# Optimization experiments

Measured on AMD Instinct MI355X. Metric: run time of the kernel, lower is better.

## Reference

```python
import jax, jax.numpy as jnp
import numpy as np

BN_EPS = 1e-5

def setup_inputs() -> dict:
    key = jax.random.key(0)
    k1, k2, k3 = jax.random.split(key, 3)
    N, F, H, E = 50000, 256, 256, 1600000
    x = jax.random.normal(k1, (N, F), dtype=jnp.float32)
    edge_index = jax.random.randint(k2, (2, E), 0, N, dtype=jnp.int64)
    # Linear(F, H) params, PyTorch default init scale
    lim = 1.0 / np.sqrt(F)
    W = jax.random.uniform(k3, (H, F), dtype=jnp.float32, minval=-lim, maxval=lim)
    b = jnp.zeros((H,), dtype=jnp.float32)
    bn_w = jnp.ones((H,), dtype=jnp.float32)
    bn_b = jnp.zeros((H,), dtype=jnp.float32)
    return {"x": x, "edge_index": edge_index, "W": W, "b": b, "bn_w": bn_w, "bn_b": bn_b}

def reference(x, edge_index, W, b, bn_w, bn_b):
    N = x.shape[0]
    src, dst = edge_index[0], edge_index[1]
    # GIN aggregation: sum of neighbor features (messages flow src -> dst)
    agg = jax.ops.segment_sum(x[src], dst, num_segments=N)
    h = x + agg  # (1 + eps) * x + agg, eps = 0
    # MLP: Linear then BatchNorm1d (training mode: batch stats, biased var)
    h = jnp.einsum('nf,hf->nh', h, W) + b
    mean = jnp.mean(h, axis=0)
    var = jnp.mean(jnp.square(h - mean), axis=0)
    out = (h - mean) * jax.lax.rsqrt(var + BN_EPS) * bn_w + bn_b
    return out
```

## Files before the change

kernel.cpp:

```cpp
#include <hip/hip_runtime.h>

#define NN 50000
#define FDIM 256
#define HDIM 256
#define BN_EPS 1e-5f
#define RB 32
#define KC 16
#define NP 264
#define SCAN_CHUNK 1024
#define NBLK_SCAN ((NN + SCAN_CHUNK - 1) / SCAN_CHUNK)

#define BKT 32
#define NBKT 1563
#define ECAP 1280
#define PFB2 1024
#define PSC_NPT 7
#define PAIR_SRC(p) (((p) >> 5) & 0xFFFFu)
#define PAIR_LDST(p) ((p) & 31u)

typedef __attribute__((ext_vector_type(8))) short short8v;
typedef __attribute__((ext_vector_type(8))) unsigned short ushort8v;
typedef __attribute__((ext_vector_type(4))) float f32x4;

__device__ __forceinline__ float b2f(unsigned short u) {
    return __uint_as_float(((unsigned)u) << 16);
}
__device__ __forceinline__ unsigned short f2b(float f) {
    unsigned u = __float_as_uint(f);
    return (unsigned short)((u + 0x7FFFu + ((u >> 16) & 1u)) >> 16);
}

__launch_bounds__(256)
__global__ void k_cvthist(const float4* __restrict__ x, const float4* __restrict__ W,
                          ushort4* __restrict__ xb, ushort4* __restrict__ Wb,
                          int nx4, int nw4,
                          const int* __restrict__ dst, int* __restrict__ bcnt, int E) {
    const int bid = blockIdx.x;
    const int t = threadIdx.x;
    if (bid < 256) {
        __shared__ int lhist[NBKT];
        int chunk = (E + 255) / 256;
        int c0 = bid * chunk;
        int c1 = min(E, c0 + chunk);
        for (int i = t; i < NBKT; i += 256) lhist[i] = 0;
        __syncthreads();
        for (int e = c0 + t; e < c1; e += 256) atomicAdd(&lhist[dst[e] >> 5], 1);
        __syncthreads();
        for (int i = t; i < NBKT; i += 256) {
            int h = lhist[i];
            if (h) atomicAdd(&bcnt[i], h);
        }
    } else {
        int i = (bid - 256) * 256 + t;
        if (i < nx4) {
            float4 v = x[i];
            xb[i] = make_ushort4(f2b(v.x), f2b(v.y), f2b(v.z), f2b(v.w));
        } else {
            int j = i - nx4;
            if (j < nw4) {
                float4 v = W[j];
                Wb[j] = make_ushort4(f2b(v.x), f2b(v.y), f2b(v.z), f2b(v.w));
            }
        }
    }
}

__global__ void k_pscan(const int* __restrict__ bcnt, int* __restrict__ bbase,
                        int* __restrict__ bcursor) {
    __shared__ int ts[256];
    int t = threadIdx.x;
    int i0 = t * PSC_NPT;
    int s = 0;
    for (int i = 0; i < PSC_NPT; i++) {
        int idx = i0 + i;
        if (idx < NBKT) s += bcnt[idx];
    }
    ts[t] = s;
    __syncthreads();
    for (int off = 1; off < 256; off <<= 1) {
        int val = (t >= off) ? ts[t - off] : 0;
        __syncthreads();
        ts[t] += val;
        __syncthreads();
    }
    int run = ts[t] - s;
    for (int i = 0; i < PSC_NPT; i++) {
        int idx = i0 + i;
        if (idx < NBKT) {
            bbase[idx] = run;
            bcursor[idx] = run;
            run += bcnt[idx];
        }
    }
}

__launch_bounds__(256)
__global__ void k_pfill(const int* __restrict__ src, const int* __restrict__ dst,
                        int* __restrict__ bcursor, unsigned int* __restrict__ pairs, int E) {
    __shared__ int lhist[NBKT];
    __shared__ int lbase[NBKT];
    int t = threadIdx.x;
    int chunk = (E + PFB2 - 1) / PFB2;
    int c0 = blockIdx.x * chunk;
    int c1 = min(E, c0 + chunk);
    for (int i = t; i < NBKT; i += 256) lhist[i] = 0;
    __syncthreads();
    for (int e = c0 + t; e < c1; e += 256) atomicAdd(&lhist[dst[e] >> 5], 1);
    __syncthreads();
    for (int i = t; i < NBKT; i += 256) {
        int h = lhist[i];
        lbase[i] = h ? atomicAdd(&bcursor[i], h) : 0;
        lhist[i] = 0;
    }
    __syncthreads();
    for (int e = c0 + t; e < c1; e += 256) {
        int d = dst[e];
        unsigned bkt = (unsigned)d >> 5;
        int rank = atomicAdd(&lhist[bkt], 1);
        pairs[lbase[bkt] + rank] = (bkt << 21) | ((unsigned)src[e] << 5) | ((unsigned)d & 31u);
    }
}

__launch_bounds__(256, 6)
__global__ void k_agg_gemm(const ushort4* __restrict__ xb4, const unsigned int* __restrict__ pairs,
                           const int* __restrict__ bbase, const int* __restrict__ bcnt,
                           const unsigned short* __restrict__ Wb, const float* __restrict__ bias,
                           unsigned short* __restrict__ hb, float* __restrict__ stat) {
    __shared__ unsigned int lp[ECAP];
    __shared__ int lhist[BKT];
    __shared__ int lofs[BKT + 1];
    __shared__ unsigned short As[BKT * NP];
    __shared__ float ssum[HDIM];
    __shared__ float ssq[HDIM];
    const int t = threadIdx.x;
    const int lane = t & 63;
    const int wid = t >> 6;
    const int q = lane >> 4;
    const int l16 = lane & 15;
    const int v0 = blockIdx.x * BKT;
    const int ebeg = bbase[blockIdx.x];
    const int ecnt = bcnt[blockIdx.x];
    const int vrows = min(BKT, NN - v0);

    ssum[t] = 0.f;
    ssq[t] = 0.f;

    if (ecnt <= ECAP) {
        if (t < BKT) lhist[t] = 0;
        __syncthreads();
        for (int e = t; e < ecnt; e += 256)
            atomicAdd(&lhist[PAIR_LDST(pairs[ebeg + e])], 1);
        __syncthreads();
        if (t == 0) {
            int run = 0;
            for (int r = 0; r < BKT; r++) { lofs[r] = run; run += lhist[r]; }
            lofs[BKT] = run;
        }
        __syncthreads();
        if (t < BKT) lhist[t] = lofs[t];
        __syncthreads();
        for (int e = t; e < ecnt; e += 256) {
            unsigned int p = pairs[ebeg + e];
            int pos = atomicAdd(&lhist[PAIR_LDST(p)], 1);
            lp[pos] = p;
        }
        __syncthreads();
#pragma unroll
        for (int i = 0; i < 8; i++) {
            int r = wid * 8 + i;
            int v = v0 + r;
            if (v < NN) {
                ushort4 u0 = xb4[(size_t)v * 64 + lane];
                float a0 = b2f(u0.x), a1 = b2f(u0.y), a2 = b2f(u0.z), a3 = b2f(u0.w);
                int e0 = __builtin_amdgcn_readfirstlane(lofs[r]);
                int e1 = __builtin_amdgcn_readfirstlane(lofs[r + 1]);
                int e = e0;
                for (; e + 16 <= e1; e += 16) {
                    ushort4 u[16];
#pragma unroll
                    for (int j = 0; j < 16; j++)
                        u[j] = xb4[(size_t)PAIR_SRC(lp[e + j]) * 64 + lane];
#pragma unroll
                    for (int j = 0; j < 16; j++) {
                        a0 += b2f(u[j].x); a1 += b2f(u[j].y);
                        a2 += b2f(u[j].z); a3 += b2f(u[j].w);
                    }
                }
                for (; e + 4 <= e1; e += 4) {
                    ushort4 ua = xb4[(size_t)PAIR_SRC(lp[e]) * 64 + lane];
                    ushort4 ub = xb4[(size_t)PAIR_SRC(lp[e + 1]) * 64 + lane];
                    ushort4 uc = xb4[(size_t)PAIR_SRC(lp[e + 2]) * 64 + lane];
                    ushort4 ud = xb4[(size_t)PAIR_SRC(lp[e + 3]) * 64 + lane];
                    a0 += (b2f(ua.x) + b2f(ub.x)) + (b2f(uc.x) + b2f(ud.x));
                    a1 += (b2f(ua.y) + b2f(ub.y)) + (b2f(uc.y) + b2f(ud.y));
                    a2 += (b2f(ua.z) + b2f(ub.z)) + (b2f(uc.z) + b2f(ud.z));
                    a3 += (b2f(ua.w) + b2f(ub.w)) + (b2f(uc.w) + b2f(ud.w));
                }
                for (; e < e1; e++) {
                    ushort4 ua = xb4[(size_t)PAIR_SRC(lp[e]) * 64 + lane];
                    a0 += b2f(ua.x); a1 += b2f(ua.y); a2 += b2f(ua.z); a3 += b2f(ua.w);
                }
                *(ushort4*)(As + r * NP + lane * 4) =
                    make_ushort4(f2b(a0), f2b(a1), f2b(a2), f2b(a3));
            } else {
                *(ushort4*)(As + r * NP + lane * 4) = make_ushort4(0, 0, 0, 0);
            }
        }
    } else {
#pragma unroll
        for (int i = 0; i < 8; i++) {
            int r = wid * 8 + i;
            int v = v0 + r;
            float a0 = 0.f, a1 = 0.f, a2 = 0.f, a3 = 0.f;
            if (v < NN) {
                ushort4 u0 = xb4[(size_t)v * 64 + lane];
                a0 = b2f(u0.x); a1 = b2f(u0.y); a2 = b2f(u0.z); a3 = b2f(u0.w);
                for (int e = 0; e < ecnt; e++) {
                    unsigned int p = pairs[ebeg + e];
                    if ((int)PAIR_LDST(p) == r) {
                        ushort4 cu = xb4[(size_t)PAIR_SRC(p) * 64 + lane];
                        a0 += b2f(cu.x); a1 += b2f(cu.y); a2 += b2f(cu.z); a3 += b2f(cu.w);
                    }
                }
            }
            *(ushort4*)(As + r * NP + lane * 4) =
                make_ushort4(f2b(a0), f2b(a1), f2b(a2), f2b(a3));
        }
    }
    __syncthreads();

    f32x4 acc[2][4];
#pragma unroll
    for (int mt = 0; mt < 2; mt++)
#pragma unroll
        for (int nt = 0; nt < 4; nt++) acc[mt][nt] = (f32x4)0.f;

    const int w = wid;
#pragma unroll
    for (int ks = 0; ks < 8; ks++) {
        const int kk = ks * 32;
        short8v af[2], bf_[4];
#pragma unroll
        for (int mt = 0; mt < 2; mt++)
            af[mt] = *(const short8v*)(As + (mt * 16 + l16) * NP + kk + q * 8);
#pragma unroll
        for (int nt = 0; nt < 4; nt++)
            bf_[nt] = *(const short8v*)(Wb + (size_t)(w * 64 + nt * 16 + l16) * FDIM + kk + q * 8);
#pragma unroll
        for (int mt = 0; mt < 2; mt++)
#pragma unroll
            for (int nt = 0; nt < 4; nt++)
                acc[mt][nt] = __builtin_amdgcn_mfma_f32_16x16x32_bf16(af[mt], bf_[nt], acc[mt][nt], 0, 0, 0);
    }

#pragma unroll
    for (int nt = 0; nt < 4; nt++) {
        const int col = w * 64 + nt * 16 + l16;
        const float bcol = bias[col];
        float s = 0.f, qq = 0.f;
#pragma unroll
        for (int mt = 0; mt < 2; mt++) {
            const int rbase = mt * 16 + q * 4;
#pragma unroll
            for (int r = 0; r < 4; r++) {
                int row = rbase + r;
                if (row < vrows) {
                    float v = acc[mt][nt][r] + bcol;
                    hb[(size_t)(v0 + row) * FDIM + col] = f2b(v);
                    s += v;
                    qq += v * v;
                }
            }
        }
        atomicAdd(&ssum[col], s);
        atomicAdd(&ssq[col], qq);
    }
    __syncthreads();
    atomicAdd(&stat[t], ssum[t]);
    atomicAdd(&stat[256 + t], ssq[t]);
}

__global__ void k_final(const float* __restrict__ stat, const float* __restrict__ bn_w,
                        const float* __restrict__ bn_b, float* __restrict__ ss) {
    int j = threadIdx.x;
    const float inv_n = 1.0f / (float)NN;
    float mean = stat[j] * inv_n;
    float var = stat[256 + j] * inv_n - mean * mean;
    float sc = bn_w[j] * rsqrtf(var + BN_EPS);
    ss[j] = sc;
    ss[256 + j] = bn_b[j] - mean * sc;
}

__global__ void k_norm8(const ushort8v* __restrict__ hb8, const float* __restrict__ ss,
                        float4* __restrict__ out, int n8) {
    int i = blockIdx.x * blockDim.x + threadIdx.x;
    if (i >= n8) return;
    ushort8v u = hb8[i];
    int c8 = (i & 31) << 3;
    float4 sc0 = *(const float4*)(ss + c8);
    float4 sc1 = *(const float4*)(ss + c8 + 4);
    float4 sh0 = *(const float4*)(ss + 256 + c8);
    float4 sh1 = *(const float4*)(ss + 256 + c8 + 4);
    float4 v0, v1;
    v0.x = fmaf(b2f(u[0]), sc0.x, sh0.x);
    v0.y = fmaf(b2f(u[1]), sc0.y, sh0.y);
    v0.z = fmaf(b2f(u[2]), sc0.z, sh0.z);
    v0.w = fmaf(b2f(u[3]), sc0.w, sh0.w);
    v1.x = fmaf(b2f(u[4]), sc1.x, sh1.x);
    v1.y = fmaf(b2f(u[5]), sc1.y, sh1.y);
    v1.z = fmaf(b2f(u[6]), sc1.z, sh1.z);
    v1.w = fmaf(b2f(u[7]), sc1.w, sh1.w);
    out[i * 2 + 0] = v0;
    out[i * 2 + 1] = v1;
}

__global__ void k_hist(const int* __restrict__ dst, int* __restrict__ cnt, int E) {
    int e = blockIdx.x * blockDim.x + threadIdx.x;
    if (e < E) atomicAdd(&cnt[dst[e]], 1);
}
__global__ void k_scan1(const int* __restrict__ cnt, int* __restrict__ offs,
                        int* __restrict__ bsum) {
    __shared__ int ts[256];
    int t = threadIdx.x;
    int base = blockIdx.x * SCAN_CHUNK + t * 4;
    int v0 = (base + 0 < NN) ? cnt[base + 0] : 0;
    int v1 = (base + 1 < NN) ? cnt[base + 1] : 0;
    int v2 = (base + 2 < NN) ? cnt[base + 2] : 0;
    int v3 = (base + 3 < NN) ? cnt[base + 3] : 0;
    int tsum = v0 + v1 + v2 + v3;
    ts[t] = tsum;
    __syncthreads();
    for (int off = 1; off < 256; off <<= 1) {
        int val = (t >= off) ? ts[t - off] : 0;
        __syncthreads();
        ts[t] += val;
        __syncthreads();
    }
    int excl = ts[t] - tsum;
    if (t == 255) bsum[blockIdx.x] = ts[255];
    if (base + 0 < NN) offs[base + 0] = excl;
    if (base + 1 < NN) offs[base + 1] = excl + v0;
    if (base + 2 < NN) offs[base + 2] = excl + v0 + v1;
    if (base + 3 < NN) offs[base + 3] = excl + v0 + v1 + v2;
}
__global__ void k_scan2(int* __restrict__ bsum, int nb) {
    __shared__ int s[64];
    int t = threadIdx.x;
    s[t] = (t < nb) ? bsum[t] : 0;
    __syncthreads();
    if (t == 0) {
        int run = 0;
        for (int i = 0; i < nb; i++) { int v = s[i]; s[i] = run; run += v; }
    }
    __syncthreads();
    if (t < nb) bsum[t] = s[t];
}
__global__ void k_scan3(int* __restrict__ offs, const int* __restrict__ bsum,
                        int* __restrict__ cursor) {
    int i = blockIdx.x * blockDim.x + threadIdx.x;
    if (i >= NN) return;
    int o = offs[i] + bsum[i >> 10];
    offs[i] = o;
    cursor[i] = o;
}
__global__ void k_bucket(const int* __restrict__ src, const int* __restrict__ dst,
                         int* __restrict__ cursor, int* __restrict__ csr, int E) {
    int e = blockIdx.x * blockDim.x + threadIdx.x;
    if (e >= E) return;
    int pos = atomicAdd(&cursor[dst[e]], 1);
    csr[pos] = src[e];
}
__global__ void k_copy(const float4* __restrict__ x, float4* __restrict__ out, int n4) {
    int i = blockIdx.x * blockDim.x + threadIdx.x;
    if (i < n4) out[i] = x[i];
}
__global__ void k_scatter(const float* __restrict__ x, const int* __restrict__ src,
                          const int* __restrict__ dst, float* __restrict__ out, int E) {
    int t = blockIdx.x * blockDim.x + threadIdx.x;
    int e = t >> 6;
    if (e >= E) return;
    int c = (t & 63) << 2;
    long s = src[e], d = dst[e];
    const float4 v = *(const float4*)(x + s * FDIM + c);
    float* o = out + d * FDIM + c;
    atomicAdd(o + 0, v.x);
    atomicAdd(o + 1, v.y);
    atomicAdd(o + 2, v.z);
    atomicAdd(o + 3, v.w);
}
__launch_bounds__(256)
__global__ void k_gather(const float4* __restrict__ x, const int* __restrict__ offs,
                         const int* __restrict__ cnt, const int* __restrict__ csr,
                         float4* __restrict__ out) {
    int v = blockIdx.x * 4 + (threadIdx.x >> 6);
    if (v >= NN) return;
    int lane = threadIdx.x & 63;
    int beg = __builtin_amdgcn_readfirstlane(offs[v]);
    int d   = __builtin_amdgcn_readfirstlane(cnt[v]);
    float4 acc = x[(size_t)v * 64 + lane];
    int i = 0;
    for (; i + 4 <= d; i += 4) {
        int s0 = csr[beg + i], s1 = csr[beg + i + 1];
        int s2 = csr[beg + i + 2], s3 = csr[beg + i + 3];
        float4 a = x[(size_t)s0 * 64 + lane];
        float4 b = x[(size_t)s1 * 64 + lane];
        float4 c = x[(size_t)s2 * 64 + lane];
        float4 e = x[(size_t)s3 * 64 + lane];
        acc.x += (a.x + b.x) + (c.x + e.x);
        acc.y += (a.y + b.y) + (c.y + e.y);
        acc.z += (a.z + b.z) + (c.z + e.z);
        acc.w += (a.w + b.w) + (c.w + e.w);
    }
    for (; i < d; i++) {
        int s = csr[beg + i];
        float4 a = x[(size_t)s * 64 + lane];
        acc.x += a.x; acc.y += a.y; acc.z += a.z; acc.w += a.w;
    }
    out[(size_t)v * 64 + lane] = acc;
}
__launch_bounds__(256)
__global__ void k_gemm_stats(float* __restrict__ h,
                             const float* __restrict__ W,
                             const float* __restrict__ bias,
                             float* __restrict__ stat) {
    __shared__ float hs[RB * FDIM];
    __shared__ float wt[KC * HDIM];
    const int j = threadIdx.x;
    const int c = j & 63;
    const int g = j >> 6;
    const long row0 = (long)blockIdx.x * RB;
    const int vrows = min(RB, NN - (int)row0);
    const int vf4 = vrows * (FDIM / 4);

    float4* hsv = (float4*)hs;
    const float4* hv = (const float4*)(h + row0 * FDIM);
#pragma unroll
    for (int i = 0; i < (RB * FDIM / 4) / 256; i++) {
        int f4 = j + i * 256;
        hsv[f4] = (f4 < vf4) ? hv[f4] : make_float4(0.f, 0.f, 0.f, 0.f);
    }
    __syncthreads();

    float acc[8][4];
#pragma unroll
    for (int r = 0; r < 8; r++)
#pragma unroll
        for (int qi = 0; qi < 4; qi++) acc[r][qi] = 0.f;

    for (int kb = 0; kb < FDIM; kb += KC) {
        __syncthreads();
#pragma unroll
        for (int i = 0; i < KC / 4; i++) {
            float4 w4 = *(const float4*)(W + (size_t)j * FDIM + kb + i * 4);
            wt[(i * 4 + 0) * HDIM + j] = w4.x;
            wt[(i * 4 + 1) * HDIM + j] = w4.y;
            wt[(i * 4 + 2) * HDIM + j] = w4.z;
            wt[(i * 4 + 3) * HDIM + j] = w4.w;
        }
        __syncthreads();
#pragma unroll
        for (int k = 0; k < KC; k++) {
            float4 wv = *(const float4*)(wt + k * HDIM + c * 4);
#pragma unroll
            for (int r = 0; r < 8; r++) {
                float hval = hs[(g * 8 + r) * FDIM + kb + k];
                acc[r][0] = fmaf(hval, wv.x, acc[r][0]);
                acc[r][1] = fmaf(hval, wv.y, acc[r][1]);
                acc[r][2] = fmaf(hval, wv.z, acc[r][2]);
                acc[r][3] = fmaf(hval, wv.w, acc[r][3]);
            }
        }
    }
    __syncthreads();
    wt[j] = 0.f;
    wt[256 + j] = 0.f;
    __syncthreads();

    float4 bv = *(const float4*)(bias + c * 4);
    float s0 = 0, s1 = 0, s2 = 0, s3 = 0, q0 = 0, q1 = 0, q2 = 0, q3 = 0;
#pragma unroll
    for (int r = 0; r < 8; r++) {
        int row = g * 8 + r;
        if (row < vrows) {
            float4 v;
            v.x = acc[r][0] + bv.x;
            v.y = acc[r][1] + bv.y;
            v.z = acc[r][2] + bv.z;
            v.w = acc[r][3] + bv.w;
            *(float4*)(h + (row0 + row) * FDIM + c * 4) = v;
            s0 += v.x; s1 += v.y; s2 += v.z; s3 += v.w;
            q0 += v.x * v.x; q1 += v.y * v.y; q2 += v.z * v.z; q3 += v.w * v.w;
        }
    }
    atomicAdd(&wt[c * 4 + 0], s0);
    atomicAdd(&wt[c * 4 + 1], s1);
    atomicAdd(&wt[c * 4 + 2], s2);
    atomicAdd(&wt[c * 4 + 3], s3);
    atomicAdd(&wt[256 + c * 4 + 0], q0);
    atomicAdd(&wt[256 + c * 4 + 1], q1);
    atomicAdd(&wt[256 + c * 4 + 2], q2);
    atomicAdd(&wt[256 + c * 4 + 3], q3);
    __syncthreads();
    atomicAdd(&stat[j], wt[j]);
    atomicAdd(&stat[256 + j], wt[256 + j]);
}
__global__ void k_norm(float* __restrict__ out, const float* __restrict__ ss, int n4) {
    int i = blockIdx.x * blockDim.x + threadIdx.x;
    if (i >= n4) return;
    float4 v = ((float4*)out)[i];
    int c4 = (i & 63) << 2;
    float4 sc = *(const float4*)(ss + c4);
    float4 sh = *(const float4*)(ss + 256 + c4);
    v.x = fmaf(v.x, sc.x, sh.x);
    v.y = fmaf(v.y, sc.y, sh.y);
    v.z = fmaf(v.z, sc.z, sh.z);
    v.w = fmaf(v.w, sc.w, sh.w);
    ((float4*)out)[i] = v;
}

extern "C" void kernel_launch(void* const* d_in, const int* in_sizes, int n_in,
                              void* d_out, int out_size, void* d_ws, size_t ws_size,
                              hipStream_t stream) {
    const float* x   = (const float*)d_in[0];
    const int*   ei  = (const int*)d_in[1];
    const float* W   = (const float*)d_in[2];
    const float* b   = (const float*)d_in[3];
    const float* bnw = (const float*)d_in[4];
    const float* bnb = (const float*)d_in[5];
    float* out = (float*)d_out;
    char* ws = (char*)d_ws;
    const int E = in_sizes[1] / 2;
    const int n4 = NN * FDIM / 4;
    const int n8 = NN * FDIM / 8;
    const int* src = ei;
    const int* dst = ei + E;

    size_t off = 0;
    float* stat = (float*)(ws + off);          off += 4096;
    int* bcnt   = (int*)(ws + off);            off += 8192;
    int* bbase  = (int*)(ws + off);            off += 8192;
    int* bcur   = (int*)(ws + off);            off += 8192;
    unsigned int* pairs = (unsigned int*)(ws + off); off += (size_t)E * 4;
    off = (off + 255) & ~(size_t)255;
    unsigned short* Wb = (unsigned short*)(ws + off); off += 131072;
    unsigned short* xb = (unsigned short*)(ws + off); off += (size_t)NN * FDIM * 2;
    unsigned short* hb = (unsigned short*)(ws + off); off += (size_t)NN * FDIM * 2;
    const size_t need_fast = off;

    size_t foff = 0;
    float* fstat  = (float*)(ws + foff); foff += 4096;
    int*   cnt    = (int*)(ws + foff);   foff += 204800;
    int*   offs   = (int*)(ws + foff);   foff += 204800;
    int*   cursor = (int*)(ws + foff);   foff += 204800;
    int*   bsum   = (int*)(ws + foff);   foff += 4096;
    int*   csr    = (int*)(ws + foff);   foff += (size_t)E * 4;
    const size_t need_mid = foff;

    const bool src_fits = (NN <= 65536);
    const int nw4 = HDIM * FDIM / 4;

    if (ws_size >= need_fast && src_fits) {
        hipMemsetAsync(ws, 0, 12288, stream);
        const int ncvt = (n4 + nw4 + 255) / 256;
        k_cvthist<<<ncvt + 256, 256, 0, stream>>>((const float4*)x, (const float4*)W,
                                                  (ushort4*)xb, (ushort4*)Wb, n4, nw4,
                                                  dst, bcnt, E);
        k_pscan<<<1, 256, 0, stream>>>(bcnt, bbase, bcur);
        k_pfill<<<PFB2, 256, 0, stream>>>(src, dst, bcur, pairs, E);
        k_agg_gemm<<<NBKT, 256, 0, stream>>>((const ushort4*)xb, pairs, bbase, bcnt,
                                             Wb, b, hb, stat);
        k_final<<<1, 256, 0, stream>>>(stat, bnw, bnb, stat + 512);
        k_norm8<<<(n8 + 255) / 256, 256, 0, stream>>>((const ushort8v*)hb, stat + 512,
                                                      (float4*)out, n8);
    } else if (ws_size >= need_mid) {
        hipMemsetAsync(fstat, 0, 2 * 256 * sizeof(float), stream);
        hipMemsetAsync(cnt, 0, NN * sizeof(int), stream);
        k_hist<<<(E + 255) / 256, 256, 0, stream>>>(dst, cnt, E);
        k_scan1<<<NBLK_SCAN, 256, 0, stream>>>(cnt, offs, bsum);
        k_scan2<<<1, 64, 0, stream>>>(bsum, NBLK_SCAN);
        k_scan3<<<(NN + 255) / 256, 256, 0, stream>>>(offs, bsum, cursor);
        k_bucket<<<(E + 255) / 256, 256, 0, stream>>>(src, dst, cursor, csr, E);
        k_gather<<<(NN + 3) / 4, 256, 0, stream>>>((const float4*)x, offs, cnt, csr,
                                                   (float4*)out);
        k_gemm_stats<<<(NN + RB - 1) / RB, 256, 0, stream>>>(out, W, b, fstat);
        k_final<<<1, 256, 0, stream>>>(fstat, bnw, bnb, fstat + 512);
        k_norm<<<(n4 + 255) / 256, 256, 0, stream>>>(out, fstat + 512, n4);
    } else {
        hipMemsetAsync(fstat, 0, 2 * 256 * sizeof(float), stream);
        k_copy<<<(n4 + 255) / 256, 256, 0, stream>>>((const float4*)x, (float4*)out, n4);
        long threads = (long)E * 64;
        k_scatter<<<(int)((threads + 255) / 256), 256, 0, stream>>>(x, src, dst, out, E);
        k_gemm_stats<<<(NN + RB - 1) / RB, 256, 0, stream>>>(out, W, b, fstat);
        k_final<<<1, 256, 0, stream>>>(fstat, bnw, bnb, fstat + 512);
        k_norm<<<(n4 + 255) / 256, 256, 0, stream>>>(out, fstat + 512, n4);
    }
}
```

Before: 340.9 us.

## Use fixed-capacity bucket slots to drop global scan and fuse stats finalize

Replaces the global histogram, single-block prefix scan and separate fill pass with one kernel. Each block sorts its edge chunk locally in shared memory and reserves space in fixed-capacity per-bucket slots (CAP per bucket) through atomics on the bucket counters. This removes two kernel launches and one full pass over dst, and turns the pair writes into coalesced runs. The BN finalize step is folded into the normalize kernel, which removes one more launch. In exchange each normalize block recomputes the scale and shift, buckets that overflow CAP fall back to scanning all E edges, and the pairs buffer grows to a fixed NBKT*CAP size.

```diff
diff --git a/kernel.cpp b/kernel.cpp
--- a/kernel.cpp
+++ b/kernel.cpp
@@ -13,7 +13,9 @@
 #define BKT 32
 #define NBKT 1563
 #define ECAP 1280
-#define PFB2 1024
+#define CAP 1280
+#define PFB3 512
+#define SBUF2 3200
 #define PSC_NPT 7
 #define PAIR_SRC(p) (((p) >> 5) & 0xFFFFu)
 #define PAIR_LDST(p) ((p) & 31u)
@@ -31,27 +33,15 @@
 }
 
 __launch_bounds__(256)
-__global__ void k_cvthist(const float4* __restrict__ x, const float4* __restrict__ W,
+__global__ void k_cvtfill(const float4* __restrict__ x, const float4* __restrict__ W,
                           ushort4* __restrict__ xb, ushort4* __restrict__ Wb,
                           int nx4, int nw4,
-                          const int* __restrict__ dst, int* __restrict__ bcnt, int E) {
+                          const int* __restrict__ src, const int* __restrict__ dst,
+                          int* __restrict__ bcnt, unsigned int* __restrict__ pairs, int E) {
     const int bid = blockIdx.x;
     const int t = threadIdx.x;
-    if (bid < 256) {
-        __shared__ int lhist[NBKT];
-        int chunk = (E + 255) / 256;
-        int c0 = bid * chunk;
-        int c1 = min(E, c0 + chunk);
-        for (int i = t; i < NBKT; i += 256) lhist[i] = 0;
-        __syncthreads();
-        for (int e = c0 + t; e < c1; e += 256) atomicAdd(&lhist[dst[e] >> 5], 1);
-        __syncthreads();
-        for (int i = t; i < NBKT; i += 256) {
-            int h = lhist[i];
-            if (h) atomicAdd(&bcnt[i], h);
-        }
-    } else {
-        int i = (bid - 256) * 256 + t;
+    if (bid >= PFB3) {
+        int i = (bid - PFB3) * 256 + t;
         if (i < nx4) {
             float4 v = x[i];
             xb[i] = make_ushort4(f2b(v.x), f2b(v.y), f2b(v.z), f2b(v.w));
@@ -62,68 +52,122 @@
                 Wb[j] = make_ushort4(f2b(v.x), f2b(v.y), f2b(v.z), f2b(v.w));
             }
         }
-    }
-}
-
-__global__ void k_pscan(const int* __restrict__ bcnt, int* __restrict__ bbase,
-                        int* __restrict__ bcursor) {
+        return;
+    }
+    __shared__ int lhist[NBKT];
+    __shared__ int lofs[NBKT];
     __shared__ int ts[256];
-    int t = threadIdx.x;
-    int i0 = t * PSC_NPT;
-    int s = 0;
-    for (int i = 0; i < PSC_NPT; i++) {
-        int idx = i0 + i;
-        if (idx < NBKT) s += bcnt[idx];
-    }
-    ts[t] = s;
-    __syncthreads();
-    for (int off = 1; off < 256; off <<= 1) {
-        int val = (t >= off) ? ts[t - off] : 0;
-        __syncthreads();
-        ts[t] += val;
-        __syncthreads();
-    }
-    int run = ts[t] - s;
-    for (int i = 0; i < PSC_NPT; i++) {
-        int idx = i0 + i;
-        if (idx < NBKT) {
-            bbase[idx] = run;
-            bcursor[idx] = run;
-            run += bcnt[idx];
-        }
-    }
-}
-
-__launch_bounds__(256)
-__global__ void k_pfill(const int* __restrict__ src, const int* __restrict__ dst,
-                        int* __restrict__ bcursor, unsigned int* __restrict__ pairs, int E) {
-    __shared__ int lhist[NBKT];
-    __shared__ int lbase[NBKT];
-    int t = threadIdx.x;
-    int chunk = (E + PFB2 - 1) / PFB2;
-    int c0 = blockIdx.x * chunk;
-    int c1 = min(E, c0 + chunk);
+    __shared__ unsigned int sbuf[SBUF2];
+    const int chunk = (E + PFB3 - 1) / PFB3;
+    const int c0 = bid * chunk;
+    const int c1 = min(E, c0 + chunk);
+    const int n = c1 - c0;
+
     for (int i = t; i < NBKT; i += 256) lhist[i] = 0;
     __syncthreads();
     for (int e = c0 + t; e < c1; e += 256) atomicAdd(&lhist[dst[e] >> 5], 1);
     __syncthreads();
-    for (int i = t; i < NBKT; i += 256) {
-        int h = lhist[i];
-        lbase[i] = h ? atomicAdd(&bcursor[i], h) : 0;
-        lhist[i] = 0;
-    }
+    {
+        int i0 = t * PSC_NPT;
+        int s = 0;
+        int loc[PSC_NPT];
+        for (int i = 0; i < PSC_NPT; i++) {
+            int idx = i0 + i;
+            loc[i] = (idx < NBKT) ? lhist[idx] : 0;
+            s += loc[i];
+        }
+        ts[t] = s;
+        __syncthreads();
+        for (int off = 1; off < 256; off <<= 1) {
+            int val = (t >= off) ? ts[t - off] : 0;
+            __syncthreads();
+            ts[t] += val;
+            __syncthreads();
+        }
+        int run = ts[t] - s;
+        for (int i = 0; i < PSC_NPT; i++) {
+            int idx = i0 + i;
+            if (idx < NBKT) {
+                lofs[idx] = run;
+                run += loc[i];
+            }
+        }
+    }
+    __syncthreads();
+    for (int i = t; i < NBKT; i += 256) lhist[i] = lofs[i];
     __syncthreads();
     for (int e = c0 + t; e < c1; e += 256) {
         int d = dst[e];
         unsigned bkt = (unsigned)d >> 5;
         int rank = atomicAdd(&lhist[bkt], 1);
-        pairs[lbase[bkt] + rank] = (bkt << 21) | ((unsigned)src[e] << 5) | ((unsigned)d & 31u);
+        sbuf[rank] = (bkt << 21) | ((unsigned)src[e] << 5) | ((unsigned)d & 31u);
+    }
+    __syncthreads();
+    for (int i = t; i < NBKT; i += 256) {
+        int cnt = lhist[i] - lofs[i];
+        int gb = cnt ? (i * CAP + atomicAdd(&bcnt[i], cnt)) : 0;
+        lhist[i] = gb - lofs[i];
+    }
+    __syncthreads();
+    for (int j = t; j < n; j += 256) {
+        unsigned int p = sbuf[j];
+        unsigned bkt = p >> 21;
+        int pos = j + lhist[bkt];
+        if (pos < (int)((bkt + 1) * CAP)) pairs[pos] = p;
+    }
+}
+
+__launch_bounds__(256)
+__global__ void k_cvtfill_d(const float4* __restrict__ x, const float4* __restrict__ W,
+                            ushort4* __restrict__ xb, ushort4* __restrict__ Wb,
+                            int nx4, int nw4,
+                            const int* __restrict__ src, const int* __restrict__ dst,
+                            int* __restrict__ bcnt, unsigned int* __restrict__ pairs, int E) {
+    const int bid = blockIdx.x;
+    const int t = threadIdx.x;
+    if (bid >= PFB3) {
+        int i = (bid - PFB3) * 256 + t;
+        if (i < nx4) {
+            float4 v = x[i];
+            xb[i] = make_ushort4(f2b(v.x), f2b(v.y), f2b(v.z), f2b(v.w));
+        } else {
+            int j = i - nx4;
+            if (j < nw4) {
+                float4 v = W[j];
+                Wb[j] = make_ushort4(f2b(v.x), f2b(v.y), f2b(v.z), f2b(v.w));
+            }
+        }
+        return;
+    }
+    __shared__ int lhist[NBKT];
+    __shared__ int lbase[NBKT];
+    const int chunk = (E + PFB3 - 1) / PFB3;
+    const int c0 = bid * chunk;
+    const int c1 = min(E, c0 + chunk);
+    for (int i = t; i < NBKT; i += 256) lhist[i] = 0;
+    __syncthreads();
+    for (int e = c0 + t; e < c1; e += 256) atomicAdd(&lhist[dst[e] >> 5], 1);
+    __syncthreads();
+    for (int i = t; i < NBKT; i += 256) {
+        int h = lhist[i];
+        lbase[i] = h ? (i * CAP + atomicAdd(&bcnt[i], h)) : 0;
+        lhist[i] = 0;
+    }
+    __syncthreads();
+    for (int e = c0 + t; e < c1; e += 256) {
+        int d = dst[e];
+        unsigned bkt = (unsigned)d >> 5;
+        int rank = atomicAdd(&lhist[bkt], 1);
+        int pos = lbase[bkt] + rank;
+        if (pos < (int)((bkt + 1) * CAP))
+            pairs[pos] = (bkt << 21) | ((unsigned)src[e] << 5) | ((unsigned)d & 31u);
     }
 }
 
 __launch_bounds__(256, 6)
 __global__ void k_agg_gemm(const ushort4* __restrict__ xb4, const unsigned int* __restrict__ pairs,
-                           const int* __restrict__ bbase, const int* __restrict__ bcnt,
+                           const int* __restrict__ bcnt,
+                           const int* __restrict__ srcv, const int* __restrict__ dstv, int E,
                            const unsigned short* __restrict__ Wb, const float* __restrict__ bias,
                            unsigned short* __restrict__ hb, float* __restrict__ stat) {
     __shared__ unsigned int lp[ECAP];
@@ -138,7 +182,7 @@
     const int q = lane >> 4;
     const int l16 = lane & 15;
     const int v0 = blockIdx.x * BKT;
-    const int ebeg = bbase[blockIdx.x];
+    const int ebeg = blockIdx.x * CAP;
     const int ecnt = bcnt[blockIdx.x];
     const int vrows = min(BKT, NN - v0);
 
@@ -215,10 +259,9 @@
             if (v < NN) {
                 ushort4 u0 = xb4[(size_t)v * 64 + lane];
                 a0 = b2f(u0.x); a1 = b2f(u0.y); a2 = b2f(u0.z); a3 = b2f(u0.w);
-                for (int e = 0; e < ecnt; e++) {
-                    unsigned int p = pairs[ebeg + e];
-                    if ((int)PAIR_LDST(p) == r) {
-                        ushort4 cu = xb4[(size_t)PAIR_SRC(p) * 64 + lane];
+                for (int e = 0; e < E; e++) {
+                    if (dstv[e] == v) {
+                        ushort4 cu = xb4[(size_t)srcv[e] * 64 + lane];
                         a0 += b2f(cu.x); a1 += b2f(cu.y); a2 += b2f(cu.z); a3 += b2f(cu.w);
                     }
                 }
@@ -280,20 +323,21 @@
     atomicAdd(&stat[256 + t], ssq[t]);
 }
 
-__global__ void k_final(const float* __restrict__ stat, const float* __restrict__ bn_w,
-                        const float* __restrict__ bn_b, float* __restrict__ ss) {
-    int j = threadIdx.x;
-    const float inv_n = 1.0f / (float)NN;
-    float mean = stat[j] * inv_n;
-    float var = stat[256 + j] * inv_n - mean * mean;
-    float sc = bn_w[j] * rsqrtf(var + BN_EPS);
-    ss[j] = sc;
-    ss[256 + j] = bn_b[j] - mean * sc;
-}
-
-__global__ void k_norm8(const ushort8v* __restrict__ hb8, const float* __restrict__ ss,
-                        float4* __restrict__ out, int n8) {
-    int i = blockIdx.x * blockDim.x + threadIdx.x;
+__global__ void k_norm8f(const ushort8v* __restrict__ hb8, const float* __restrict__ stat,
+                         const float* __restrict__ bn_w, const float* __restrict__ bn_b,
+                         float4* __restrict__ out, int n8) {
+    __shared__ float ss[512];
+    const int t = threadIdx.x;
+    {
+        const float inv_n = 1.0f / (float)NN;
+        float mean = stat[t] * inv_n;
+        float var = stat[256 + t] * inv_n - mean * mean;
+        float sc = bn_w[t] * rsqrtf(var + BN_EPS);
+        ss[t] = sc;
+        ss[256 + t] = bn_b[t] - mean * sc;
+    }
+    __syncthreads();
+    int i = blockIdx.x * 256 + t;
     if (i >= n8) return;
     ushort8v u = hb8[i];
     int c8 = (i & 31) << 3;
@@ -314,6 +358,16 @@
     out[i * 2 + 1] = v1;
 }
 
+__global__ void k_final(const float* __restrict__ stat, const float* __restrict__ bn_w,
+                        const float* __restrict__ bn_b, float* __restrict__ ss) {
+    int j = threadIdx.x;
+    const float inv_n = 1.0f / (float)NN;
+    float mean = stat[j] * inv_n;
+    float var = stat[256 + j] * inv_n - mean * mean;
+    float sc = bn_w[j] * rsqrtf(var + BN_EPS);
+    ss[j] = sc;
+    ss[256 + j] = bn_b[j] - mean * sc;
+}
 __global__ void k_hist(const int* __restrict__ dst, int* __restrict__ cnt, int E) {
     int e = blockIdx.x * blockDim.x + threadIdx.x;
     if (e < E) atomicAdd(&cnt[dst[e]], 1);
@@ -538,9 +592,7 @@
     size_t off = 0;
     float* stat = (float*)(ws + off);          off += 4096;
     int* bcnt   = (int*)(ws + off);            off += 8192;
-    int* bbase  = (int*)(ws + off);            off += 8192;
-    int* bcur   = (int*)(ws + off);            off += 8192;
-    unsigned int* pairs = (unsigned int*)(ws + off); off += (size_t)E * 4;
+    unsigned int* pairs = (unsigned int*)(ws + off); off += (size_t)NBKT * CAP * 4;
     off = (off + 255) & ~(size_t)255;
     unsigned short* Wb = (unsigned short*)(ws + off); off += 131072;
     unsigned short* xb = (unsigned short*)(ws + off); off += (size_t)NN * FDIM * 2;
@@ -562,16 +614,19 @@
     if (ws_size >= need_fast && src_fits) {
         hipMemsetAsync(ws, 0, 12288, stream);
         const int ncvt = (n4 + nw4 + 255) / 256;
-        k_cvthist<<<ncvt + 256, 256, 0, stream>>>((const float4*)x, (const float4*)W,
-                                                  (ushort4*)xb, (ushort4*)Wb, n4, nw4,
-                                                  dst, bcnt, E);
-        k_pscan<<<1, 256, 0, stream>>>(bcnt, bbase, bcur);
-        k_pfill<<<PFB2, 256, 0, stream>>>(src, dst, bcur, pairs, E);
-        k_agg_gemm<<<NBKT, 256, 0, stream>>>((const ushort4*)xb, pairs, bbase, bcnt,
-                                             Wb, b, hb, stat);
-        k_final<<<1, 256, 0, stream>>>(stat, bnw, bnb, stat + 512);
-        k_norm8<<<(n8 + 255) / 256, 256, 0, stream>>>((const ushort8v*)hb, stat + 512,
-                                                      (float4*)out, n8);
+        const int chunk = (E + PFB3 - 1) / PFB3;
+        if (chunk <= SBUF2)
+            k_cvtfill<<<PFB3 + ncvt, 256, 0, stream>>>((const float4*)x, (const float4*)W,
+                                                       (ushort4*)xb, (ushort4*)Wb, n4, nw4,
+                                                       src, dst, bcnt, pairs, E);
+        else
+            k_cvtfill_d<<<PFB3 + ncvt, 256, 0, stream>>>((const float4*)x, (const float4*)W,
+                                                         (ushort4*)xb, (ushort4*)Wb, n4, nw4,
+                                                         src, dst, bcnt, pairs, E);
+        k_agg_gemm<<<NBKT, 256, 0, stream>>>((const ushort4*)xb, pairs, bcnt,
+                                             src, dst, E, Wb, b, hb, stat);
+        k_norm8f<<<(n8 + 255) / 256, 256, 0, stream>>>((const ushort8v*)hb, stat,
+                                                       bnw, bnb, (float4*)out, n8);
     } else if (ws_size >= need_mid) {
         hipMemsetAsync(fstat, 0, 2 * 256 * sizeof(float), stream);
         hipMemsetAsync(cnt, 0, NN * sizeof(int), stream);
```

Result: faster. 296.1 us (-13.1%).

## Replace bucket sort with fixed-capacity per-node adjacency slots and fuse BN finalize

Applied to the files above, without the earlier changes.

Drops the histogram, prefix-scan and pair-fill passes. Each edge now atomically claims a slot in a fixed-capacity (96) per-destination array of 16-bit source ids, done inside the conversion kernel. The aggregation kernel copies those slots straight into shared memory, and the BN scale/shift computation moves into the normalize kernel. This removes three launches and the sort traffic, at the cost of global atomics on per-node counters, a larger padded workspace, and a very slow full-edge-scan fallback for any node whose degree exceeds the capacity.

```diff
diff --git a/kernel.cpp b/kernel.cpp
--- a/kernel.cpp
+++ b/kernel.cpp
@@ -12,11 +12,8 @@
 
 #define BKT 32
 #define NBKT 1563
-#define ECAP 1280
-#define PFB2 1024
-#define PSC_NPT 7
-#define PAIR_SRC(p) (((p) >> 5) & 0xFFFFu)
-#define PAIR_LDST(p) ((p) & 31u)
+#define NNP (NBKT * BKT)
+#define CAPN 96
 
 typedef __attribute__((ext_vector_type(8))) short short8v;
 typedef __attribute__((ext_vector_type(8))) unsigned short ushort8v;
@@ -31,104 +28,44 @@
 }
 
 __launch_bounds__(256)
-__global__ void k_cvthist(const float4* __restrict__ x, const float4* __restrict__ W,
-                          ushort4* __restrict__ xb, ushort4* __restrict__ Wb,
-                          int nx4, int nw4,
-                          const int* __restrict__ dst, int* __restrict__ bcnt, int E) {
+__global__ void k_cvtfill2(const float4* __restrict__ x, const float4* __restrict__ W,
+                           ushort4* __restrict__ xb, ushort4* __restrict__ Wb,
+                           int nx4, int nw4,
+                           const int* __restrict__ src, const int* __restrict__ dst,
+                           int* __restrict__ ncnt, unsigned short* __restrict__ prs,
+                           int E, int nfb) {
     const int bid = blockIdx.x;
     const int t = threadIdx.x;
-    if (bid < 256) {
-        __shared__ int lhist[NBKT];
-        int chunk = (E + 255) / 256;
-        int c0 = bid * chunk;
-        int c1 = min(E, c0 + chunk);
-        for (int i = t; i < NBKT; i += 256) lhist[i] = 0;
-        __syncthreads();
-        for (int e = c0 + t; e < c1; e += 256) atomicAdd(&lhist[dst[e] >> 5], 1);
-        __syncthreads();
-        for (int i = t; i < NBKT; i += 256) {
-            int h = lhist[i];
-            if (h) atomicAdd(&bcnt[i], h);
-        }
+    if (bid < nfb) {
+        int e = bid * 256 + t;
+        if (e < E) {
+            int d = dst[e];
+            int pos = atomicAdd(&ncnt[d], 1);
+            if (pos < CAPN) prs[(size_t)d * CAPN + pos] = (unsigned short)src[e];
+        }
+        return;
+    }
+    int i = (bid - nfb) * 256 + t;
+    if (i < nx4) {
+        float4 v = x[i];
+        xb[i] = make_ushort4(f2b(v.x), f2b(v.y), f2b(v.z), f2b(v.w));
     } else {
-        int i = (bid - 256) * 256 + t;
-        if (i < nx4) {
-            float4 v = x[i];
-            xb[i] = make_ushort4(f2b(v.x), f2b(v.y), f2b(v.z), f2b(v.w));
-        } else {
-            int j = i - nx4;
-            if (j < nw4) {
-                float4 v = W[j];
-                Wb[j] = make_ushort4(f2b(v.x), f2b(v.y), f2b(v.z), f2b(v.w));
-            }
-        }
-    }
-}
-
-__global__ void k_pscan(const int* __restrict__ bcnt, int* __restrict__ bbase,
-                        int* __restrict__ bcursor) {
-    __shared__ int ts[256];
-    int t = threadIdx.x;
-    int i0 = t * PSC_NPT;
-    int s = 0;
-    for (int i = 0; i < PSC_NPT; i++) {
-        int idx = i0 + i;
-        if (idx < NBKT) s += bcnt[idx];
-    }
-    ts[t] = s;
-    __syncthreads();
-    for (int off = 1; off < 256; off <<= 1) {
-        int val = (t >= off) ? ts[t - off] : 0;
-        __syncthreads();
-        ts[t] += val;
-        __syncthreads();
-    }
-    int run = ts[t] - s;
-    for (int i = 0; i < PSC_NPT; i++) {
-        int idx = i0 + i;
-        if (idx < NBKT) {
-            bbase[idx] = run;
-            bcursor[idx] = run;
-            run += bcnt[idx];
-        }
-    }
-}
-
-__launch_bounds__(256)
-__global__ void k_pfill(const int* __restrict__ src, const int* __restrict__ dst,
-                        int* __restrict__ bcursor, unsigned int* __restrict__ pairs, int E) {
-    __shared__ int lhist[NBKT];
-    __shared__ int lbase[NBKT];
-    int t = threadIdx.x;
-    int chunk = (E + PFB2 - 1) / PFB2;
-    int c0 = blockIdx.x * chunk;
-    int c1 = min(E, c0 + chunk);
-    for (int i = t; i < NBKT; i += 256) lhist[i] = 0;
-    __syncthreads();
-    for (int e = c0 + t; e < c1; e += 256) atomicAdd(&lhist[dst[e] >> 5], 1);
-    __syncthreads();
-    for (int i = t; i < NBKT; i += 256) {
-        int h = lhist[i];
-        lbase[i] = h ? atomicAdd(&bcursor[i], h) : 0;
-        lhist[i] = 0;
-    }
-    __syncthreads();
-    for (int e = c0 + t; e < c1; e += 256) {
-        int d = dst[e];
-        unsigned bkt = (unsigned)d >> 5;
-        int rank = atomicAdd(&lhist[bkt], 1);
-        pairs[lbase[bkt] + rank] = (bkt << 21) | ((unsigned)src[e] << 5) | ((unsigned)d & 31u);
+        int j = i - nx4;
+        if (j < nw4) {
+            float4 v = W[j];
+            Wb[j] = make_ushort4(f2b(v.x), f2b(v.y), f2b(v.z), f2b(v.w));
+        }
     }
 }
 
 __launch_bounds__(256, 6)
-__global__ void k_agg_gemm(const ushort4* __restrict__ xb4, const unsigned int* __restrict__ pairs,
-                           const int* __restrict__ bbase, const int* __restrict__ bcnt,
+__global__ void k_agg_gemm(const ushort4* __restrict__ xb4, const unsigned short* __restrict__ prs,
+                           const int* __restrict__ ncnt,
+                           const int* __restrict__ srcv, const int* __restrict__ dstv, int E,
                            const unsigned short* __restrict__ Wb, const float* __restrict__ bias,
                            unsigned short* __restrict__ hb, float* __restrict__ stat) {
-    __shared__ unsigned int lp[ECAP];
-    __shared__ int lhist[BKT];
-    __shared__ int lofs[BKT + 1];
+    __shared__ unsigned short lp[BKT * CAPN];
+    __shared__ int lcnt[BKT];
     __shared__ unsigned short As[BKT * NP];
     __shared__ float ssum[HDIM];
     __shared__ float ssq[HDIM];
@@ -138,48 +75,36 @@
     const int q = lane >> 4;
     const int l16 = lane & 15;
     const int v0 = blockIdx.x * BKT;
-    const int ebeg = bbase[blockIdx.x];
-    const int ecnt = bcnt[blockIdx.x];
     const int vrows = min(BKT, NN - v0);
 
     ssum[t] = 0.f;
     ssq[t] = 0.f;
-
-    if (ecnt <= ECAP) {
-        if (t < BKT) lhist[t] = 0;
-        __syncthreads();
-        for (int e = t; e < ecnt; e += 256)
-            atomicAdd(&lhist[PAIR_LDST(pairs[ebeg + e])], 1);
-        __syncthreads();
-        if (t == 0) {
-            int run = 0;
-            for (int r = 0; r < BKT; r++) { lofs[r] = run; run += lhist[r]; }
-            lofs[BKT] = run;
-        }
-        __syncthreads();
-        if (t < BKT) lhist[t] = lofs[t];
-        __syncthreads();
-        for (int e = t; e < ecnt; e += 256) {
-            unsigned int p = pairs[ebeg + e];
-            int pos = atomicAdd(&lhist[PAIR_LDST(p)], 1);
-            lp[pos] = p;
-        }
-        __syncthreads();
-#pragma unroll
-        for (int i = 0; i < 8; i++) {
-            int r = wid * 8 + i;
-            int v = v0 + r;
-            if (v < NN) {
-                ushort4 u0 = xb4[(size_t)v * 64 + lane];
-                float a0 = b2f(u0.x), a1 = b2f(u0.y), a2 = b2f(u0.z), a3 = b2f(u0.w);
-                int e0 = __builtin_amdgcn_readfirstlane(lofs[r]);
-                int e1 = __builtin_amdgcn_readfirstlane(lofs[r + 1]);
-                int e = e0;
+    if (t < BKT) lcnt[t] = ncnt[v0 + t];
+    {
+        const int* gp = (const int*)(prs + (size_t)v0 * CAPN);
+        int* lpi = (int*)lp;
+#pragma unroll
+        for (int i = 0; i < (BKT * CAPN / 2) / 256; i++)
+            lpi[t + i * 256] = gp[t + i * 256];
+    }
+    __syncthreads();
+
+#pragma unroll
+    for (int i = 0; i < 8; i++) {
+        int r = wid * 8 + i;
+        int v = v0 + r;
+        if (v < NN) {
+            const int cnt = __builtin_amdgcn_readfirstlane(lcnt[r]);
+            ushort4 u0 = xb4[(size_t)v * 64 + lane];
+            float a0 = b2f(u0.x), a1 = b2f(u0.y), a2 = b2f(u0.z), a3 = b2f(u0.w);
+            if (cnt <= CAPN) {
+                int e = r * CAPN;
+                const int e1 = e + cnt;
                 for (; e + 16 <= e1; e += 16) {
                     ushort4 u[16];
 #pragma unroll
                     for (int j = 0; j < 16; j++)
-                        u[j] = xb4[(size_t)PAIR_SRC(lp[e + j]) * 64 + lane];
+                        u[j] = xb4[(size_t)lp[e + j] * 64 + lane];
 #pragma unroll
                     for (int j = 0; j < 16; j++) {
                         a0 += b2f(u[j].x); a1 += b2f(u[j].y);
@@ -187,44 +112,31 @@
                     }
                 }
                 for (; e + 4 <= e1; e += 4) {
-                    ushort4 ua = xb4[(size_t)PAIR_SRC(lp[e]) * 64 + lane];
-                    ushort4 ub = xb4[(size_t)PAIR_SRC(lp[e + 1]) * 64 + lane];
-                    ushort4 uc = xb4[(size_t)PAIR_SRC(lp[e + 2]) * 64 + lane];
-                    ushort4 ud = xb4[(size_t)PAIR_SRC(lp[e + 3]) * 64 + lane];
+                    ushort4 ua = xb4[(size_t)lp[e] * 64 + lane];
+                    ushort4 ub = xb4[(size_t)lp[e + 1] * 64 + lane];
+                    ushort4 uc = xb4[(size_t)lp[e + 2] * 64 + lane];
+                    ushort4 ud = xb4[(size_t)lp[e + 3] * 64 + lane];
                     a0 += (b2f(ua.x) + b2f(ub.x)) + (b2f(uc.x) + b2f(ud.x));
                     a1 += (b2f(ua.y) + b2f(ub.y)) + (b2f(uc.y) + b2f(ud.y));
                     a2 += (b2f(ua.z) + b2f(ub.z)) + (b2f(uc.z) + b2f(ud.z));
                     a3 += (b2f(ua.w) + b2f(ub.w)) + (b2f(uc.w) + b2f(ud.w));
                 }
                 for (; e < e1; e++) {
-                    ushort4 ua = xb4[(size_t)PAIR_SRC(lp[e]) * 64 + lane];
+                    ushort4 ua = xb4[(size_t)lp[e] * 64 + lane];
                     a0 += b2f(ua.x); a1 += b2f(ua.y); a2 += b2f(ua.z); a3 += b2f(ua.w);
                 }
-                *(ushort4*)(As + r * NP + lane * 4) =
-                    make_ushort4(f2b(a0), f2b(a1), f2b(a2), f2b(a3));
             } else {
-                *(ushort4*)(As + r * NP + lane * 4) = make_ushort4(0, 0, 0, 0);
-            }
-        }
-    } else {
-#pragma unroll
-        for (int i = 0; i < 8; i++) {
-            int r = wid * 8 + i;
-            int v = v0 + r;
-            float a0 = 0.f, a1 = 0.f, a2 = 0.f, a3 = 0.f;
-            if (v < NN) {
-                ushort4 u0 = xb4[(size_t)v * 64 + lane];
-                a0 = b2f(u0.x); a1 = b2f(u0.y); a2 = b2f(u0.z); a3 = b2f(u0.w);
-                for (int e = 0; e < ecnt; e++) {
-                    unsigned int p = pairs[ebeg + e];
-                    if ((int)PAIR_LDST(p) == r) {
-                        ushort4 cu = xb4[(size_t)PAIR_SRC(p) * 64 + lane];
+                for (int e = 0; e < E; e++) {
+                    if (dstv[e] == v) {
+                        ushort4 cu = xb4[(size_t)srcv[e] * 64 + lane];
                         a0 += b2f(cu.x); a1 += b2f(cu.y); a2 += b2f(cu.z); a3 += b2f(cu.w);
                     }
                 }
             }
             *(ushort4*)(As + r * NP + lane * 4) =
                 make_ushort4(f2b(a0), f2b(a1), f2b(a2), f2b(a3));
+        } else {
+            *(ushort4*)(As + r * NP + lane * 4) = make_ushort4(0, 0, 0, 0);
         }
     }
     __syncthreads();
@@ -280,20 +192,21 @@
     atomicAdd(&stat[256 + t], ssq[t]);
 }
 
-__global__ void k_final(const float* __restrict__ stat, const float* __restrict__ bn_w,
-                        const float* __restrict__ bn_b, float* __restrict__ ss) {
-    int j = threadIdx.x;
-    const float inv_n = 1.0f / (float)NN;
-    float mean = stat[j] * inv_n;
-    float var = stat[256 + j] * inv_n - mean * mean;
-    float sc = bn_w[j] * rsqrtf(var + BN_EPS);
-    ss[j] = sc;
-    ss[256 + j] = bn_b[j] - mean * sc;
-}
-
-__global__ void k_norm8(const ushort8v* __restrict__ hb8, const float* __restrict__ ss,
-                        float4* __restrict__ out, int n8) {
-    int i = blockIdx.x * blockDim.x + threadIdx.x;
+__global__ void k_norm8f(const ushort8v* __restrict__ hb8, const float* __restrict__ stat,
+                         const float* __restrict__ bn_w, const float* __restrict__ bn_b,
+                         float4* __restrict__ out, int n8) {
+    __shared__ float ss[512];
+    const int t = threadIdx.x;
+    {
+        const float inv_n = 1.0f / (float)NN;
+        float mean = stat[t] * inv_n;
+        float var = stat[256 + t] * inv_n - mean * mean;
+        float sc = bn_w[t] * rsqrtf(var + BN_EPS);
+        ss[t] = sc;
+        ss[256 + t] = bn_b[t] - mean * sc;
+    }
+    __syncthreads();
+    int i = blockIdx.x * 256 + t;
     if (i >= n8) return;
     ushort8v u = hb8[i];
     int c8 = (i & 31) << 3;
@@ -314,6 +227,16 @@
     out[i * 2 + 1] = v1;
 }
 
+__global__ void k_final(const float* __restrict__ stat, const float* __restrict__ bn_w,
+                        const float* __restrict__ bn_b, float* __restrict__ ss) {
+    int j = threadIdx.x;
+    const float inv_n = 1.0f / (float)NN;
+    float mean = stat[j] * inv_n;
+    float var = stat[256 + j] * inv_n - mean * mean;
+    float sc = bn_w[j] * rsqrtf(var + BN_EPS);
+    ss[j] = sc;
+    ss[256 + j] = bn_b[j] - mean * sc;
+}
 __global__ void k_hist(const int* __restrict__ dst, int* __restrict__ cnt, int E) {
     int e = blockIdx.x * blockDim.x + threadIdx.x;
     if (e < E) atomicAdd(&cnt[dst[e]], 1);
@@ -537,10 +460,9 @@
 
     size_t off = 0;
     float* stat = (float*)(ws + off);          off += 4096;
-    int* bcnt   = (int*)(ws + off);            off += 8192;
-    int* bbase  = (int*)(ws + off);            off += 8192;
-    int* bcur   = (int*)(ws + off);            off += 8192;
-    unsigned int* pairs = (unsigned int*)(ws + off); off += (size_t)E * 4;
+    int* ncnt   = (int*)(ws + off);            off += 204800;
+    unsigned short* prs = (unsigned short*)(ws + off);
+    off += (size_t)NNP * CAPN * 2;
     off = (off + 255) & ~(size_t)255;
     unsigned short* Wb = (unsigned short*)(ws + off); off += 131072;
     unsigned short* xb = (unsigned short*)(ws + off); off += (size_t)NN * FDIM * 2;
@@ -560,18 +482,16 @@
     const int nw4 = HDIM * FDIM / 4;
 
     if (ws_size >= need_fast && src_fits) {
-        hipMemsetAsync(ws, 0, 12288, stream);
+        hipMemsetAsync(ws, 0, 208896, stream);
+        const int nfb = (E + 255) / 256;
         const int ncvt = (n4 + nw4 + 255) / 256;
-        k_cvthist<<<ncvt + 256, 256, 0, stream>>>((const float4*)x, (const float4*)W,
-                                                  (ushort4*)xb, (ushort4*)Wb, n4, nw4,
-                                                  dst, bcnt, E);
-        k_pscan<<<1, 256, 0, stream>>>(bcnt, bbase, bcur);
-        k_pfill<<<PFB2, 256, 0, stream>>>(src, dst, bcur, pairs, E);
-        k_agg_gemm<<<NBKT, 256, 0, stream>>>((const ushort4*)xb, pairs, bbase, bcnt,
-                                             Wb, b, hb, stat);
-        k_final<<<1, 256, 0, stream>>>(stat, bnw, bnb, stat + 512);
-        k_norm8<<<(n8 + 255) / 256, 256, 0, stream>>>((const ushort8v*)hb, stat + 512,
-                                                      (float4*)out, n8);
+        k_cvtfill2<<<nfb + ncvt, 256, 0, stream>>>((const float4*)x, (const float4*)W,
+                                                   (ushort4*)xb, (ushort4*)Wb, n4, nw4,
+                                                   src, dst, ncnt, prs, E, nfb);
+        k_agg_gemm<<<NBKT, 256, 0, stream>>>((const ushort4*)xb, prs, ncnt,
+                                             src, dst, E, Wb, b, hb, stat);
+        k_norm8f<<<(n8 + 255) / 256, 256, 0, stream>>>((const ushort8v*)hb, stat,
+                                                       bnw, bnb, (float4*)out, n8);
     } else if (ws_size >= need_mid) {
         hipMemsetAsync(fstat, 0, 2 * 256 * sizeof(float), stream);
         hipMemsetAsync(cnt, 0, NN * sizeof(int), stream);
```

After: 409.3 us. 20.0% more time.
